# Kernel optimization log

Measured on AMD Instinct MI355X. Metric: run time of the kernel, lower is better.

Reference implementation:

```python
import jax, jax.numpy as jnp
import numpy as np

B, T, S, D, L, V = 32, 64, 128, 512, 2, 32000
DSRC = 2 * D  # bidirectional encoder
PAD = 1


def setup_inputs() -> dict:
    key = jax.random.key(0)
    ks = jax.random.split(key, 16)
    sc = 0.05
    embed = jax.random.normal(ks[5], (V, D), jnp.float32) * sc
    embed = embed.at[PAD].set(0.0)  # padding_idx row is zero
    return {
        "prev_tgt_tokens": jax.random.randint(ks[0], (B, T), 0, V),
        "encoder_out": jax.random.normal(ks[1], (B, S, DSRC), jnp.float32),
        "hiddens": jax.random.normal(ks[2], (L, B, D), jnp.float32) * sc,
        "cells": jax.random.normal(ks[3], (L, B, D), jnp.float32) * sc,
        "src_mask": jax.random.randint(ks[4], (B, S), 0, 2).astype(bool),
        "embed": embed,
        "W_ih": jax.random.normal(ks[6], (L, 4 * D, D), jnp.float32) * sc,
        "W_hh": jax.random.normal(ks[7], (L, 4 * D, D), jnp.float32) * sc,
        "b_ih": jnp.zeros((L, 4 * D), jnp.float32),
        "b_hh": jnp.zeros((L, 4 * D), jnp.float32),
        "W_in": jax.random.normal(ks[8], (DSRC, D), jnp.float32) * sc,   # input_proj: d_tgt -> d_src
        "b_in": jnp.zeros((DSRC,), jnp.float32),
        "W_out": jax.random.normal(ks[9], (D, DSRC + D), jnp.float32) * sc,  # out_proj
        "b_out": jnp.zeros((D,), jnp.float32),
    }


def reference(prev_tgt_tokens, encoder_out, hiddens, cells, src_mask,
              embed, W_ih, W_hh, b_ih, b_hh, W_in, b_in, W_out, b_out):
    n_layers, _, d_model = hiddens.shape
    tgt_len = prev_tgt_tokens.shape[1]
    tgt_embed = embed[prev_tgt_tokens]          # [B, T, D]
    xs = jnp.swapaxes(tgt_embed, 0, 1)          # [T, B, D]

    def lstm_cell(x, h, c, l):
        gates = x @ W_ih[l].T + b_ih[l] + h @ W_hh[l].T + b_hh[l]  # [B, 4D]
        i, f, g, o = jnp.split(gates, 4, axis=-1)
        c2 = jax.nn.sigmoid(f) * c + jax.nn.sigmoid(i) * jnp.tanh(g)
        h2 = jax.nn.sigmoid(o) * jnp.tanh(c2)
        return h2, c2

    def step(h_carry, y_t):
        s = y_t
        new_h = []
        for l in range(n_layers):
            h2, c2 = lstm_cell(s, h_carry[l], cells[l], l)
            # Faithful to source bug: `prev_hiddens[l], prev_hiddens[l] = (hidden, cell)`
            # stores the NEW CELL into the hidden slot; prev_cells never updated.
            new_h.append(c2)
            s = h2
        # attention
        xq = s @ W_in.T + b_in                              # [B, DSRC]
        e = jnp.einsum('bsd,bd->bs', encoder_out, xq)       # [B, S]
        e = jnp.where(src_mask, -1e9, e)
        attn = jax.nn.softmax(e, axis=-1)
        ctx = jnp.einsum('bs,bsd->bd', attn, encoder_out)   # [B, DSRC]
        out_t = jnp.tanh(jnp.concatenate([ctx, s], axis=-1) @ W_out.T + b_out)
        return jnp.stack(new_h), out_t

    _, outs = jax.lax.scan(step, hiddens, xs)   # outs: [T, B, D]
    # faithful to torch.cat(outs, dim=0).view(-1, tgt_len, d_model)
    return outs.reshape(-1, d_model).reshape(-1, tgt_len, d_model)
```

## Files before the change

kernel.cpp:

```cpp
#include <hip/hip_runtime.h>
#include <math.h>

typedef unsigned short u16;
typedef __attribute__((ext_vector_type(4))) float f4;
typedef __attribute__((ext_vector_type(4))) unsigned short us4;
typedef __attribute__((ext_vector_type(8))) unsigned short us8;
typedef __attribute__((ext_vector_type(8))) short bfrag;
typedef __attribute__((ext_vector_type(4))) float f32x4;

#define BB 32
#define TT 64
#define DD 512
#define G4_ 2048

__device__ __forceinline__ float sigf(float x) { return 1.0f / (1.0f + expf(-x)); }
__device__ __forceinline__ float bf2f(u16 u) {
    union { unsigned int i; float f; } v; v.i = ((unsigned int)u) << 16; return v.f;
}
__device__ __forceinline__ u16 f2bf(float f) {
    union { float f; unsigned int i; } v; v.f = f;
    unsigned int r = v.i + 0x7fffu + ((v.i >> 16) & 1u);
    return (u16)(r >> 16);
}

__global__ void k_flag(const unsigned char* __restrict__ m, int* __restrict__ flag) {
    int tid = threadIdx.x;
    int badbyte = 0, nonz_off = 0, evenu16_nz = 0;
    for (int i = tid * 16; i < tid * 16 + 16; i++) {
        unsigned char c = m[i];
        if (c > 1) badbyte = 1;
        if ((i & 3) != 0 && c != 0) nonz_off = 1;
    }
    const u16* mu = (const u16*)m;
    for (int i = tid * 8; i < tid * 8 + 8; i++) {
        if ((i & 1) == 0 && mu[i] != 0) evenu16_nz = 1;
    }
    __shared__ int s_bad, s_noff, s_env;
    if (tid == 0) { s_bad = 0; s_noff = 0; s_env = 0; }
    __syncthreads();
    if (badbyte) atomicOr(&s_bad, 1);
    if (nonz_off) atomicOr(&s_noff, 1);
    if (evenu16_nz) atomicOr(&s_env, 1);
    __syncthreads();
    if (tid == 0) {
        int f;
        if (s_bad) f = s_env ? 2 : 3;
        else       f = s_noff ? 0 : 1;
        *flag = f;
    }
}

__global__ void __launch_bounds__(256) k_init2(const float* __restrict__ hid,
                                               u16* __restrict__ h0s,
                                               u16* __restrict__ h1s) {
    int i = blockIdx.x * 256 + threadIdx.x;
    u16 v0 = f2bf(hid[i]), v1 = f2bf(hid[16384 + i]);
    h0s[i] = v0; h0s[16384 + i] = v0;
    h1s[i] = v1; h1s[16384 + i] = v1;
}

__global__ void __launch_bounds__(256) k_packAll(const float* __restrict__ Wih,
                                                 const float* __restrict__ Whh,
                                                 const float* __restrict__ Win,
                                                 const float* __restrict__ Wout,
                                                 u16* __restrict__ wpin,
                                                 u16* __restrict__ wpout,
                                                 u16* __restrict__ wih0p,
                                                 u16* __restrict__ php) {
    const int blk = blockIdx.x;
    const int tid = threadIdx.x;
    const float* sp;
    u16* dst;
    if (blk < 256) {
        int g = blk * 256 + tid;
        int lane = g & 63, grp = g >> 6;
        int j16 = grp >> 4, ks = grp & 15;
        sp = &Win[((size_t)(j16 * 16 + (lane & 15))) * 512 + ks * 32 + (lane >> 4) * 8];
        dst = &wpin[(size_t)g * 8];
    } else if (blk < 640) {
        int g = (blk - 256) * 256 + tid;
        int lane = g & 63, grp = g >> 6;
        int j16 = grp / 48, ks = grp % 48;
        sp = &Wout[((size_t)(j16 * 16 + (lane & 15))) * 1536 + ks * 32 + (lane >> 4) * 8];
        dst = &wpout[(size_t)g * 8];
    } else if (blk < 1152) {
        int g = (blk - 640) * 256 + tid;
        int lane = g & 63, grp = g >> 6;
        int j16 = grp >> 4, ks = grp & 15;
        sp = &Wih[((size_t)(j16 * 16 + (lane & 15))) * 512 + ks * 32 + (lane >> 4) * 8];
        dst = &wih0p[(size_t)g * 8];
    } else {
        int gidx = (blk - 1152) * 256 + tid;
        int m = gidx >> 17;
        int rem = gidx & 131071;
        int lane = rem & 63;
        int q = rem >> 6;
        int ks = q & 15, T = q >> 4;
        int g = T >> 5, d16 = T & 31;
        int j = g * 512 + d16 * 16 + (lane & 15);
        int kcol = ks * 32 + (lane >> 4) * 8;
        const float* src = (m == 0) ? Whh
                         : (m == 1) ? (Wih + 1048576)
                                    : (Whh + 1048576);
        sp = &src[(size_t)j * 512 + kcol];
        dst = &php[((size_t)m << 20) + (size_t)rem * 8];
    }
    f4 v0 = *(const f4*)&sp[0];
    f4 v1 = *(const f4*)&sp[4];
    dst[0] = f2bf(v0[0]); dst[1] = f2bf(v0[1]); dst[2] = f2bf(v0[2]); dst[3] = f2bf(v0[3]);
    dst[4] = f2bf(v1[0]); dst[5] = f2bf(v1[1]); dst[6] = f2bf(v1[2]); dst[7] = f2bf(v1[3]);
}

__global__ void __launch_bounds__(256) k_gih0_mfma(const int* __restrict__ tokens,
                                                   const float* __restrict__ embed,
                                                   const u16* __restrict__ Wp,
                                                   const float* __restrict__ bih,
                                                   const float* __restrict__ bhh,
                                                   float* __restrict__ gih0p) {
    const int tid = threadIdx.x;
    const int lane = tid & 63, w = tid >> 6;
    const int t = blockIdx.y;
    const int jw = blockIdx.x * 256 + w * 64;
    __shared__ u16 xs[32][520];
    __shared__ int toks[32];
    if (tid < 32) toks[tid] = tokens[tid * TT + t];
    __syncthreads();
    for (int i = tid; i < 32 * 128; i += 256) {
        int b = i >> 7, k4 = i & 127;
        f4 v = *(const f4*)&embed[(size_t)toks[b] * 512 + k4 * 4];
        u16* dst = &xs[b][k4 * 4];
        dst[0] = f2bf(v[0]); dst[1] = f2bf(v[1]); dst[2] = f2bf(v[2]); dst[3] = f2bf(v[3]);
    }
    __syncthreads();

    const int l15 = lane & 15, l4 = lane >> 4;
    f32x4 acc[2][4];
#pragma unroll
    for (int mi = 0; mi < 2; mi++)
#pragma unroll
        for (int ni = 0; ni < 4; ni++) acc[mi][ni] = (f32x4){0.f, 0.f, 0.f, 0.f};

    for (int ks = 0; ks < 16; ks++) {
        bfrag a0 = *(const bfrag*)&xs[l15][ks * 32 + l4 * 8];
        bfrag a1 = *(const bfrag*)&xs[16 + l15][ks * 32 + l4 * 8];
#pragma unroll
        for (int ni = 0; ni < 4; ni++) {
            int j16 = (jw + ni * 16) >> 4;
            bfrag bf = *(const bfrag*)&Wp[(((size_t)j16 * 16 + ks) * 64 + lane) * 8];
            acc[0][ni] = __builtin_amdgcn_mfma_f32_16x16x32_bf16(a0, bf, acc[0][ni], 0, 0, 0);
            acc[1][ni] = __builtin_amdgcn_mfma_f32_16x16x32_bf16(a1, bf, acc[1][ni], 0, 0, 0);
        }
    }

#pragma unroll
    for (int ni = 0; ni < 4; ni++) {
        int j16 = (jw >> 4) + ni;
        int g = j16 >> 5, d16 = j16 & 31;
        int j = j16 * 16 + l15;
        float bv = bih[j] + bhh[j];
#pragma unroll
        for (int mi = 0; mi < 2; mi++) {
            f32x4 sv = acc[mi][ni];
            sv[0] += bv; sv[1] += bv; sv[2] += bv; sv[3] += bv;
            *(f32x4*)&gih0p[(((((size_t)t * 32 + d16) * 4 + g) * 2 + mi) * 64 + lane) * 4] = sv;
        }
    }
}

__global__ void __launch_bounds__(256) k_phaseM(
    const int k,
    const float* __restrict__ gih0p,
    const u16* __restrict__ whh0p,
    const u16* __restrict__ wih1p,
    const u16* __restrict__ whh1p,
    const float* __restrict__ bih1,
    const float* __restrict__ bhh1,
    const float* __restrict__ cells,
    const u16* __restrict__ h0r, u16* __restrict__ h0w,
    const u16* __restrict__ h20r, u16* __restrict__ h20w,
    const u16* __restrict__ h1r, u16* __restrict__ h1w,
    u16* __restrict__ H2)
{
    const int tid = threadIdx.x;
    const int lane = tid & 63, w = tid >> 6;
    const int l15 = lane & 15, l4 = lane >> 4;
    const int unitL = w >> 1, sub = w & 1;
    __shared__ u16 xsA[32][520];
    __shared__ u16 xsB[32][520];
    __shared__ float red[2][4][64][4];

    if (blockIdx.x < 32) {
        if (k >= 64) return;
        const int d16mi = blockIdx.x * 2 + unitL;
        const int d16 = d16mi >> 1, mi = d16mi & 1;
        const int d = d16 * 16 + l15;
        f32x4 acc[4];
#pragma unroll
        for (int g = 0; g < 4; g++) {
            if (sub == 0)
                acc[g] = *(const f32x4*)&gih0p[(((((size_t)k * 32 + d16) * 4 + g) * 2 + mi) * 64 + lane) * 4];
            else
                acc[g] = (f32x4){0.f, 0.f, 0.f, 0.f};
        }
        for (int i = tid; i < 2048; i += 256) {
            int b = i >> 6, k8 = i & 63;
            *(us8*)&xsA[b][k8 * 8] = *(const us8*)&h0r[b * 512 + k8 * 8];
        }
        __syncthreads();
        const int arow = mi * 16 + l15;
        const int ks0 = sub * 8;
        for (int ks = ks0; ks < ks0 + 8; ks++) {
            bfrag a = *(const bfrag*)&xsA[arow][ks * 32 + l4 * 8];
#pragma unroll
            for (int g = 0; g < 4; g++) {
                int T = g * 32 + d16;
                bfrag bf = *(const bfrag*)&whh0p[(((size_t)T * 16 + ks) * 64 + lane) * 8];
                acc[g] = __builtin_amdgcn_mfma_f32_16x16x32_bf16(a, bf, acc[g], 0, 0, 0);
            }
        }
        if (sub == 1) {
#pragma unroll
            for (int g = 0; g < 4; g++)
                *(f32x4*)&red[unitL][g][lane][0] = acc[g];
        }
        __syncthreads();
        if (sub == 0) {
#pragma unroll
            for (int g = 0; g < 4; g++) {
                f32x4 pv = *(const f32x4*)&red[unitL][g][lane][0];
                acc[g][0] += pv[0]; acc[g][1] += pv[1]; acc[g][2] += pv[2]; acc[g][3] += pv[3];
            }
#pragma unroll
            for (int r = 0; r < 4; r++) {
                int b = mi * 16 + l4 * 4 + r;
                float gi = acc[0][r];
                float gf = acc[1][r];
                float gg = acc[2][r];
                float go = acc[3][r];
                float cell = cells[b * 512 + d];
                float c2 = sigf(gf) * cell + sigf(gi) * tanhf(gg);
                float h2 = sigf(go) * tanhf(c2);
                h0w[b * 512 + d] = f2bf(c2);
                h20w[b * 512 + d] = f2bf(h2);
            }
        }
    } else {
        if (k < 1) return;
        for (int i = tid; i < 2048; i += 256) {
            int b = i >> 6, k8 = i & 63;
            *(us8*)&xsA[b][k8 * 8] = *(const us8*)&h20r[b * 512 + k8 * 8];
            *(us8*)&xsB[b][k8 * 8] = *(const us8*)&h1r[b * 512 + k8 * 8];
        }
        __syncthreads();
        const int d16mi = (blockIdx.x - 32) * 2 + unitL;
        const int d16 = d16mi >> 1, mi = d16mi & 1;
        const int d = d16 * 16 + l15;
        const int arow = mi * 16 + l15;
        const u16 (* __restrict__ xsrc)[520] = sub ? xsB : xsA;
        const u16* wsrc = sub ? whh1p : wih1p;
        f32x4 acc[4];
#pragma unroll
        for (int g = 0; g < 4; g++) acc[g] = (f32x4){0.f, 0.f, 0.f, 0.f};
        for (int ks = 0; ks < 16; ks++) {
            bfrag a = *(const bfrag*)&xsrc[arow][ks * 32 + l4 * 8];
#pragma unroll
            for (int g = 0; g < 4; g++) {
                int T = g * 32 + d16;
                bfrag bf = *(const bfrag*)&wsrc[(((size_t)T * 16 + ks) * 64 + lane) * 8];
                acc[g] = __builtin_amdgcn_mfma_f32_16x16x32_bf16(a, bf, acc[g], 0, 0, 0);
            }
        }
        if (sub == 1) {
#pragma unroll
            for (int g = 0; g < 4; g++)
                *(f32x4*)&red[unitL][g][lane][0] = acc[g];
        }
        __syncthreads();
        if (sub == 0) {
#pragma unroll
            for (int g = 0; g < 4; g++) {
                f32x4 pv = *(const f32x4*)&red[unitL][g][lane][0];
                acc[g][0] += pv[0]; acc[g][1] += pv[1]; acc[g][2] += pv[2]; acc[g][3] += pv[3];
            }
            float bb0 = bih1[0 * 512 + d] + bhh1[0 * 512 + d];
            float bb1v = bih1[1 * 512 + d] + bhh1[1 * 512 + d];
            float bb2 = bih1[2 * 512 + d] + bhh1[2 * 512 + d];
            float bb3 = bih1[3 * 512 + d] + bhh1[3 * 512 + d];
#pragma unroll
            for (int r = 0; r < 4; r++) {
                int b = mi * 16 + l4 * 4 + r;
                float gi = acc[0][r] + bb0;
                float gf = acc[1][r] + bb1v;
                float gg = acc[2][r] + bb2;
                float go = acc[3][r] + bb3;
                float cell = cells[16384 + b * 512 + d];
                float c2 = sigf(gf) * cell + sigf(gi) * tanhf(gg);
                float h2 = sigf(go) * tanhf(c2);
                h1w[b * 512 + d] = f2bf(c2);
                H2[(size_t)(k - 1) * 16384 + b * 512 + d] = f2bf(h2);
            }
        }
    }
}

__global__ void __launch_bounds__(256) k_x_mfma(const u16* __restrict__ H2,
                                                const u16* __restrict__ Wpin,
                                                const float* __restrict__ bin,
                                                u16* __restrict__ XQ) {
    const int tid = threadIdx.x;
    const int lane = tid & 63, w = tid >> 6;
    const int t = blockIdx.y;
    const int jw = blockIdx.x * 256 + w * 64;
    __shared__ u16 xs[32][520];
    for (int i = tid; i < 2048; i += 256) {
        int b = i >> 6, k8 = i & 63;
        *(us8*)&xs[b][k8 * 8] = *(const us8*)&H2[(size_t)t * 16384 + b * 512 + k8 * 8];
    }
    __syncthreads();
    const int l15 = lane & 15, l4 = lane >> 4;
    f32x4 acc[2][4];
#pragma unroll
    for (int mi = 0; mi < 2; mi++)
#pragma unroll
        for (int ni = 0; ni < 4; ni++) acc[mi][ni] = (f32x4){0.f, 0.f, 0.f, 0.f};
    for (int ks = 0; ks < 16; ks++) {
        bfrag a0 = *(const bfrag*)&xs[l15][ks * 32 + l4 * 8];
        bfrag a1 = *(const bfrag*)&xs[16 + l15][ks * 32 + l4 * 8];
#pragma unroll
        for (int ni = 0; ni < 4; ni++) {
            int j16 = (jw + ni * 16) >> 4;
            bfrag bf = *(const bfrag*)&Wpin[(((size_t)j16 * 16 + ks) * 64 + lane) * 8];
            acc[0][ni] = __builtin_amdgcn_mfma_f32_16x16x32_bf16(a0, bf, acc[0][ni], 0, 0, 0);
            acc[1][ni] = __builtin_amdgcn_mfma_f32_16x16x32_bf16(a1, bf, acc[1][ni], 0, 0, 0);
        }
    }
#pragma unroll
    for (int ni = 0; ni < 4; ni++) {
        int j = jw + ni * 16 + l15;
        float bv = bin[j];
#pragma unroll
        for (int mi = 0; mi < 2; mi++) {
#pragma unroll
            for (int r = 0; r < 4; r++) {
                int b = mi * 16 + l4 * 4 + r;
                XQ[((size_t)(t * 32 + b)) * 1024 + j] = f2bf(acc[mi][ni][r] + bv);
            }
        }
    }
}

__global__ void __launch_bounds__(256) k_out_mfma(const u16* __restrict__ CTX,
                                                  const u16* __restrict__ H2,
                                                  const u16* __restrict__ Wpout,
                                                  const float* __restrict__ bout,
                                                  float* __restrict__ out) {
    const int tid = threadIdx.x;
    const int lane = tid & 63, w = tid >> 6;
    const int t = blockIdx.y;
    const int jw = blockIdx.x * 256 + w * 64;
    __shared__ u16 xs[32][520];
    const int l15 = lane & 15, l4 = lane >> 4;
    f32x4 acc[2][4];
#pragma unroll
    for (int mi = 0; mi < 2; mi++)
#pragma unroll
        for (int ni = 0; ni < 4; ni++) acc[mi][ni] = (f32x4){0.f, 0.f, 0.f, 0.f};
    for (int c = 0; c < 3; c++) {
        if (c) __syncthreads();
        if (c < 2) {
            for (int i = tid; i < 2048; i += 256) {
                int b = i >> 6, k8 = i & 63;
                *(us8*)&xs[b][k8 * 8] = *(const us8*)&CTX[((size_t)(t * 32 + b)) * 1024 + c * 512 + k8 * 8];
            }
        } else {
            for (int i = tid; i < 2048; i += 256) {
                int b = i >> 6, k8 = i & 63;
                *(us8*)&xs[b][k8 * 8] = *(const us8*)&H2[(size_t)t * 16384 + b * 512 + k8 * 8];
            }
        }
        __syncthreads();
        for (int ks = 0; ks < 16; ks++) {
            bfrag a0 = *(const bfrag*)&xs[l15][ks * 32 + l4 * 8];
            bfrag a1 = *(const bfrag*)&xs[16 + l15][ks * 32 + l4 * 8];
#pragma unroll
            for (int ni = 0; ni < 4; ni++) {
                int j16 = (jw + ni * 16) >> 4;
                bfrag bf = *(const bfrag*)&Wpout[(((size_t)j16 * 48 + c * 16 + ks) * 64 + lane) * 8];
                acc[0][ni] = __builtin_amdgcn_mfma_f32_16x16x32_bf16(a0, bf, acc[0][ni], 0, 0, 0);
                acc[1][ni] = __builtin_amdgcn_mfma_f32_16x16x32_bf16(a1, bf, acc[1][ni], 0, 0, 0);
            }
        }
    }
#pragma unroll
    for (int ni = 0; ni < 4; ni++) {
        int j = jw + ni * 16 + l15;
        float bv = bout[j];
#pragma unroll
        for (int mi = 0; mi < 2; mi++) {
#pragma unroll
            for (int r = 0; r < 4; r++) {
                int b = mi * 16 + l4 * 4 + r;
                out[((size_t)(t * 32 + b)) * 512 + j] = tanhf(acc[mi][ni][r] + bv);
            }
        }
    }
}

__global__ void __launch_bounds__(256) k_att8(const u16* __restrict__ XQ,
                                              const float* __restrict__ enc,
                                              const unsigned char* __restrict__ mask,
                                              const int* __restrict__ flag,
                                              u16* __restrict__ CTX) {
    const int tid = threadIdx.x;
    const int b = blockIdx.x, t0 = blockIdx.y * 8;
    __shared__ float xq[8][1024];
    __shared__ float ered[8][256];
    __shared__ float attn[8][128];
    __shared__ float red2[8][8];
#pragma unroll
    for (int tg = 0; tg < 8; tg++) {
        us4 v = *(const us4*)&XQ[((size_t)((t0 + tg) * 32 + b)) * 1024 + tid * 4];
        float* dst = &xq[tg][tid * 4];
        dst[0] = bf2f(v[0]); dst[1] = bf2f(v[1]); dst[2] = bf2f(v[2]); dst[3] = bf2f(v[3]);
    }
    __syncthreads();
    const int s = tid >> 1, hh = tid & 1;
    float p[8] = {0.f, 0.f, 0.f, 0.f, 0.f, 0.f, 0.f, 0.f};
    const float* erow = enc + ((size_t)(b * 128 + s)) * 1024 + hh * 512;
    for (int k4 = 0; k4 < 128; k4++) {
        f4 u = *(const f4*)&erow[k4 * 4];
#pragma unroll
        for (int kk = 0; kk < 4; kk++) {
#pragma unroll
            for (int tg = 0; tg < 8; tg++)
                p[tg] += u[kk] * xq[tg][hh * 512 + k4 * 4 + kk];
        }
    }
#pragma unroll
    for (int tg = 0; tg < 8; tg++) ered[tg][tid] = p[tg];
    __syncthreads();
    bool msk = false;
    if (tid < 128) {
        int f = *flag;
        if (f == 0)      msk = mask[b * 128 + tid] != 0;
        else if (f == 1) msk = ((const int*)mask)[b * 128 + tid] != 0;
        else if (f == 2) msk = ((const u16*)mask)[b * 128 + tid] != 0;
        else             msk = ((const unsigned int*)mask)[b * 128 + tid] != 0;
    }
    const int wave = tid >> 6;
    float e[8];
#pragma unroll
    for (int tg = 0; tg < 8; tg++) {
        e[tg] = -INFINITY;
        if (tid < 128) {
            e[tg] = ered[tg][2 * tid] + ered[tg][2 * tid + 1];
            if (msk) e[tg] = -1e9f;
        }
        float v = e[tg];
#pragma unroll
        for (int off = 32; off >= 1; off >>= 1) v = fmaxf(v, __shfl_xor(v, off));
        if ((tid & 63) == 0) red2[tg][wave] = v;
    }
    __syncthreads();
#pragma unroll
    for (int tg = 0; tg < 8; tg++) {
        float mx = fmaxf(fmaxf(red2[tg][0], red2[tg][1]), fmaxf(red2[tg][2], red2[tg][3]));
        float pp = (tid < 128) ? expf(e[tg] - mx) : 0.f;
        float su = pp;
#pragma unroll
        for (int off = 32; off >= 1; off >>= 1) su += __shfl_xor(su, off);
        if ((tid & 63) == 0) red2[tg][4 + wave] = su;
        __syncthreads();
        float S = (red2[tg][4] + red2[tg][5]) + (red2[tg][6] + red2[tg][7]);
        if (tid < 128) attn[tg][tid] = pp / S;
        __syncthreads();
    }
    float c0[8] = {0}, c1[8] = {0}, c2v[8] = {0}, c3[8] = {0};
    const float* eb = enc + ((size_t)b * 128) * 1024 + tid * 4;
    for (int s2 = 0; s2 < 128; s2++) {
        f4 u = *(const f4*)&eb[(size_t)s2 * 1024];
#pragma unroll
        for (int tg = 0; tg < 8; tg++) {
            float a = attn[tg][s2];
            c0[tg] += a * u[0]; c1[tg] += a * u[1]; c2v[tg] += a * u[2]; c3[tg] += a * u[3];
        }
    }
#pragma unroll
    for (int tg = 0; tg < 8; tg++) {
        u16* crow = CTX + ((size_t)((t0 + tg) * 32 + b)) * 1024 + tid * 4;
        crow[0] = f2bf(c0[tg]); crow[1] = f2bf(c1[tg]);
        crow[2] = f2bf(c2v[tg]); crow[3] = f2bf(c3[tg]);
    }
}

extern "C" void kernel_launch(void* const* d_in, const int* in_sizes, int n_in,
                              void* d_out, int out_size, void* d_ws, size_t ws_size,
                              hipStream_t stream) {
    const int* tokens   = (const int*)d_in[0];
    const float* enc    = (const float*)d_in[1];
    const float* hidden = (const float*)d_in[2];
    const float* cells  = (const float*)d_in[3];
    const unsigned char* mask = (const unsigned char*)d_in[4];
    const float* embed  = (const float*)d_in[5];
    const float* W_ih   = (const float*)d_in[6];
    const float* W_hh   = (const float*)d_in[7];
    const float* b_ih   = (const float*)d_in[8];
    const float* b_hh   = (const float*)d_in[9];
    const float* W_in   = (const float*)d_in[10];
    const float* b_in   = (const float*)d_in[11];
    const float* W_out  = (const float*)d_in[12];
    const float* b_out  = (const float*)d_in[13];
    float* out = (float*)d_out;

    float* ws = (float*)d_ws;
    float* gih0p = ws;
    u16*   h0s  = (u16*)(ws + 4194304);
    u16*   h20s = (u16*)(ws + 4210688);
    u16*   h1s  = (u16*)(ws + 4227072);
    u16*   H2   = (u16*)(ws + 4243456);
    u16*   php  = (u16*)(ws + 4767744);
    u16*   whh0p = php;
    u16*   wih1p = php + 1048576;
    u16*   whh1p = php + 2097152;
    u16*   wpin  = (u16*)(ws + 6340608);
    u16*   wpout = (u16*)(ws + 6602752);
    u16*   wih0p = (u16*)(ws + 6995968);
    int*   flag  = (int*)(ws + 7520256);
    u16*   XQ   = (u16*)ws;
    u16*   CTX  = (u16*)(ws + 1048576);

    const float* bih1 = b_ih + G4_;
    const float* bhh1 = b_hh + G4_;

    k_flag<<<1, 256, 0, stream>>>(mask, flag);
    k_init2<<<64, 256, 0, stream>>>(hidden, h0s, h1s);
    k_packAll<<<2688, 256, 0, stream>>>(W_ih, W_hh, W_in, W_out, wpin, wpout, wih0p, php);
    k_gih0_mfma<<<dim3(8, 64), 256, 0, stream>>>(tokens, embed, wih0p, b_ih, b_hh, gih0p);

    for (int k = 0; k <= 64; k++) {
        const int r = k & 1, w = r ^ 1;
        k_phaseM<<<64, 256, 0, stream>>>(k, gih0p, whh0p, wih1p, whh1p, bih1, bhh1, cells,
                                         h0s + r * 16384, h0s + w * 16384,
                                         h20s + r * 16384, h20s + w * 16384,
                                         h1s + r * 16384, h1s + w * 16384, H2);
    }

    k_x_mfma<<<dim3(4, 64), 256, 0, stream>>>(H2, wpin, b_in, XQ);
    k_att8<<<dim3(32, 8), 256, 0, stream>>>(XQ, enc, mask, flag, CTX);
    k_out_mfma<<<dim3(2, 64), 256, 0, stream>>>(CTX, H2, wpout, b_out, out);
}
```

Before: 593.9 us.

## Split attention into MFMA QK-softmax and AV kernels with bf16 encoder tiles

Replaces the scalar fp32 attention kernel with two bf16 MFMA kernels. One computes scores for 32 timesteps per block, applies the mask and softmax, and writes bf16 attention weights to workspace. The other multiplies those weights by a transposed bf16 encoder tile to produce the context. The goal is to move the attention dot products onto matrix cores. The cost is an extra launch, an intermediate buffer round trip, and bf16 rounding of the encoder values and attention weights.

```diff
diff --git a/kernel.cpp b/kernel.cpp
--- a/kernel.cpp
+++ b/kernel.cpp
@@ -349,6 +349,146 @@
     }
 }
 
+__global__ void __launch_bounds__(256) k_qk_mfma(const u16* __restrict__ XQ,
+                                                 const float* __restrict__ enc,
+                                                 const unsigned char* __restrict__ mask,
+                                                 const int* __restrict__ flag,
+                                                 u16* __restrict__ ATT) {
+    const int tid = threadIdx.x;
+    const int lane = tid & 63, w = tid >> 6;
+    const int l15 = lane & 15, l4 = lane >> 4;
+    const int b = blockIdx.x, th = blockIdx.y;
+    __shared__ u16 qs[32][136];
+    __shared__ u16 encC[128][136];
+    __shared__ float es[32][132];
+    f32x4 acc[2][2];
+#pragma unroll
+    for (int mt = 0; mt < 2; mt++)
+#pragma unroll
+        for (int ni = 0; ni < 2; ni++) acc[mt][ni] = (f32x4){0.f, 0.f, 0.f, 0.f};
+
+    for (int dc = 0; dc < 8; dc++) {
+        if (dc) __syncthreads();
+        for (int i = tid; i < 512; i += 256) {
+            int tr = i >> 4, k8 = i & 15;
+            *(us8*)&qs[tr][k8 * 8] =
+                *(const us8*)&XQ[((size_t)((th * 32 + tr) * 32 + b)) * 1024 + dc * 128 + k8 * 8];
+        }
+        for (int i = tid; i < 4096; i += 256) {
+            int s = i >> 5, d4 = i & 31;
+            f4 v = *(const f4*)&enc[((size_t)(b * 128 + s)) * 1024 + dc * 128 + d4 * 4];
+            u16* dst = &encC[s][d4 * 4];
+            dst[0] = f2bf(v[0]); dst[1] = f2bf(v[1]); dst[2] = f2bf(v[2]); dst[3] = f2bf(v[3]);
+        }
+        __syncthreads();
+        for (int ks = 0; ks < 4; ks++) {
+            bfrag a0 = *(const bfrag*)&qs[l15][ks * 32 + l4 * 8];
+            bfrag a1 = *(const bfrag*)&qs[16 + l15][ks * 32 + l4 * 8];
+#pragma unroll
+            for (int ni = 0; ni < 2; ni++) {
+                int nt = w * 2 + ni;
+                bfrag bf = *(const bfrag*)&encC[nt * 16 + l15][ks * 32 + l4 * 8];
+                acc[0][ni] = __builtin_amdgcn_mfma_f32_16x16x32_bf16(a0, bf, acc[0][ni], 0, 0, 0);
+                acc[1][ni] = __builtin_amdgcn_mfma_f32_16x16x32_bf16(a1, bf, acc[1][ni], 0, 0, 0);
+            }
+        }
+    }
+    __syncthreads();
+#pragma unroll
+    for (int mt = 0; mt < 2; mt++) {
+#pragma unroll
+        for (int ni = 0; ni < 2; ni++) {
+            int nt = w * 2 + ni;
+#pragma unroll
+            for (int r = 0; r < 4; r++)
+                es[mt * 16 + l4 * 4 + r][nt * 16 + l15] = acc[mt][ni][r];
+        }
+    }
+    __syncthreads();
+    const int row = tid >> 3, seg = tid & 7;
+    int f = *flag;
+    float p[16];
+    float mx = -INFINITY;
+#pragma unroll
+    for (int j = 0; j < 16; j++) {
+        int col = seg * 16 + j;
+        bool msk;
+        if (f == 0)      msk = mask[b * 128 + col] != 0;
+        else if (f == 1) msk = ((const int*)mask)[b * 128 + col] != 0;
+        else if (f == 2) msk = ((const u16*)mask)[b * 128 + col] != 0;
+        else             msk = ((const unsigned int*)mask)[b * 128 + col] != 0;
+        float e = es[row][col];
+        if (msk) e = -1e9f;
+        p[j] = e;
+        mx = fmaxf(mx, e);
+    }
+#pragma unroll
+    for (int off = 4; off >= 1; off >>= 1) mx = fmaxf(mx, __shfl_xor(mx, off));
+    float su = 0.f;
+#pragma unroll
+    for (int j = 0; j < 16; j++) { p[j] = expf(p[j] - mx); su += p[j]; }
+#pragma unroll
+    for (int off = 4; off >= 1; off >>= 1) su += __shfl_xor(su, off);
+    u16* arow = &ATT[((size_t)(b * 64 + th * 32 + row)) * 128 + seg * 16];
+#pragma unroll
+    for (int j = 0; j < 16; j++) arow[j] = f2bf(p[j] / su);
+}
+
+__global__ void __launch_bounds__(256) k_av_mfma(const u16* __restrict__ ATT,
+                                                 const float* __restrict__ enc,
+                                                 u16* __restrict__ CTX) {
+    const int tid = threadIdx.x;
+    const int lane = tid & 63, w = tid >> 6;
+    const int l15 = lane & 15, l4 = lane >> 4;
+    const int b = blockIdx.x, nc = blockIdx.y;
+    __shared__ u16 as_[64][136];
+    __shared__ u16 encT[256][136];
+    for (int i = tid; i < 1024; i += 256) {
+        int tr = i >> 4, k8 = i & 15;
+        *(us8*)&as_[tr][k8 * 8] = *(const us8*)&ATT[((size_t)(b * 64 + tr)) * 128 + k8 * 8];
+    }
+    for (int i = tid; i < 8192; i += 256) {
+        int d4 = i & 63, s = i >> 6;
+        f4 v = *(const f4*)&enc[((size_t)(b * 128 + s)) * 1024 + nc * 256 + d4 * 4];
+        encT[d4 * 4 + 0][s] = f2bf(v[0]);
+        encT[d4 * 4 + 1][s] = f2bf(v[1]);
+        encT[d4 * 4 + 2][s] = f2bf(v[2]);
+        encT[d4 * 4 + 3][s] = f2bf(v[3]);
+    }
+    __syncthreads();
+    f32x4 acc[4][4];
+#pragma unroll
+    for (int mt = 0; mt < 4; mt++)
+#pragma unroll
+        for (int ni = 0; ni < 4; ni++) acc[mt][ni] = (f32x4){0.f, 0.f, 0.f, 0.f};
+    for (int ks = 0; ks < 4; ks++) {
+        bfrag a[4];
+#pragma unroll
+        for (int mt = 0; mt < 4; mt++)
+            a[mt] = *(const bfrag*)&as_[mt * 16 + l15][ks * 32 + l4 * 8];
+#pragma unroll
+        for (int ni = 0; ni < 4; ni++) {
+            int nt = w * 4 + ni;
+            bfrag bf = *(const bfrag*)&encT[nt * 16 + l15][ks * 32 + l4 * 8];
+#pragma unroll
+            for (int mt = 0; mt < 4; mt++)
+                acc[mt][ni] = __builtin_amdgcn_mfma_f32_16x16x32_bf16(a[mt], bf, acc[mt][ni], 0, 0, 0);
+        }
+    }
+#pragma unroll
+    for (int ni = 0; ni < 4; ni++) {
+        int n = nc * 256 + (w * 4 + ni) * 16 + l15;
+#pragma unroll
+        for (int mt = 0; mt < 4; mt++) {
+#pragma unroll
+            for (int r = 0; r < 4; r++) {
+                int t = mt * 16 + l4 * 4 + r;
+                CTX[((size_t)(t * 32 + b)) * 1024 + n] = f2bf(acc[mt][ni][r]);
+            }
+        }
+    }
+}
+
 __global__ void __launch_bounds__(256) k_out_mfma(const u16* __restrict__ CTX,
                                                   const u16* __restrict__ H2,
                                                   const u16* __restrict__ Wpout,
@@ -403,93 +543,6 @@
                 out[((size_t)(t * 32 + b)) * 512 + j] = tanhf(acc[mi][ni][r] + bv);
             }
         }
-    }
-}
-
-__global__ void __launch_bounds__(256) k_att8(const u16* __restrict__ XQ,
-                                              const float* __restrict__ enc,
-                                              const unsigned char* __restrict__ mask,
-                                              const int* __restrict__ flag,
-                                              u16* __restrict__ CTX) {
-    const int tid = threadIdx.x;
-    const int b = blockIdx.x, t0 = blockIdx.y * 8;
-    __shared__ float xq[8][1024];
-    __shared__ float ered[8][256];
-    __shared__ float attn[8][128];
-    __shared__ float red2[8][8];
-#pragma unroll
-    for (int tg = 0; tg < 8; tg++) {
-        us4 v = *(const us4*)&XQ[((size_t)((t0 + tg) * 32 + b)) * 1024 + tid * 4];
-        float* dst = &xq[tg][tid * 4];
-        dst[0] = bf2f(v[0]); dst[1] = bf2f(v[1]); dst[2] = bf2f(v[2]); dst[3] = bf2f(v[3]);
-    }
-    __syncthreads();
-    const int s = tid >> 1, hh = tid & 1;
-    float p[8] = {0.f, 0.f, 0.f, 0.f, 0.f, 0.f, 0.f, 0.f};
-    const float* erow = enc + ((size_t)(b * 128 + s)) * 1024 + hh * 512;
-    for (int k4 = 0; k4 < 128; k4++) {
-        f4 u = *(const f4*)&erow[k4 * 4];
-#pragma unroll
-        for (int kk = 0; kk < 4; kk++) {
-#pragma unroll
-            for (int tg = 0; tg < 8; tg++)
-                p[tg] += u[kk] * xq[tg][hh * 512 + k4 * 4 + kk];
-        }
-    }
-#pragma unroll
-    for (int tg = 0; tg < 8; tg++) ered[tg][tid] = p[tg];
-    __syncthreads();
-    bool msk = false;
-    if (tid < 128) {
-        int f = *flag;
-        if (f == 0)      msk = mask[b * 128 + tid] != 0;
-        else if (f == 1) msk = ((const int*)mask)[b * 128 + tid] != 0;
-        else if (f == 2) msk = ((const u16*)mask)[b * 128 + tid] != 0;
-        else             msk = ((const unsigned int*)mask)[b * 128 + tid] != 0;
-    }
-    const int wave = tid >> 6;
-    float e[8];
-#pragma unroll
-    for (int tg = 0; tg < 8; tg++) {
-        e[tg] = -INFINITY;
-        if (tid < 128) {
-            e[tg] = ered[tg][2 * tid] + ered[tg][2 * tid + 1];
-            if (msk) e[tg] = -1e9f;
-        }
-        float v = e[tg];
-#pragma unroll
-        for (int off = 32; off >= 1; off >>= 1) v = fmaxf(v, __shfl_xor(v, off));
-        if ((tid & 63) == 0) red2[tg][wave] = v;
-    }
-    __syncthreads();
-#pragma unroll
-    for (int tg = 0; tg < 8; tg++) {
-        float mx = fmaxf(fmaxf(red2[tg][0], red2[tg][1]), fmaxf(red2[tg][2], red2[tg][3]));
-        float pp = (tid < 128) ? expf(e[tg] - mx) : 0.f;
-        float su = pp;
-#pragma unroll
-        for (int off = 32; off >= 1; off >>= 1) su += __shfl_xor(su, off);
-        if ((tid & 63) == 0) red2[tg][4 + wave] = su;
-        __syncthreads();
-        float S = (red2[tg][4] + red2[tg][5]) + (red2[tg][6] + red2[tg][7]);
-        if (tid < 128) attn[tg][tid] = pp / S;
-        __syncthreads();
-    }
-    float c0[8] = {0}, c1[8] = {0}, c2v[8] = {0}, c3[8] = {0};
-    const float* eb = enc + ((size_t)b * 128) * 1024 + tid * 4;
-    for (int s2 = 0; s2 < 128; s2++) {
-        f4 u = *(const f4*)&eb[(size_t)s2 * 1024];
-#pragma unroll
-        for (int tg = 0; tg < 8; tg++) {
-            float a = attn[tg][s2];
-            c0[tg] += a * u[0]; c1[tg] += a * u[1]; c2v[tg] += a * u[2]; c3[tg] += a * u[3];
-        }
-    }
-#pragma unroll
-    for (int tg = 0; tg < 8; tg++) {
-        u16* crow = CTX + ((size_t)((t0 + tg) * 32 + b)) * 1024 + tid * 4;
-        crow[0] = f2bf(c0[tg]); crow[1] = f2bf(c1[tg]);
-        crow[2] = f2bf(c2v[tg]); crow[3] = f2bf(c3[tg]);
     }
 }
 
@@ -528,6 +581,7 @@
     int*   flag  = (int*)(ws + 7520256);
     u16*   XQ   = (u16*)ws;
     u16*   CTX  = (u16*)(ws + 1048576);
+    u16*   ATT  = (u16*)(ws + 2097152);
 
     const float* bih1 = b_ih + G4_;
     const float* bhh1 = b_hh + G4_;
@@ -546,6 +600,7 @@
     }
 
     k_x_mfma<<<dim3(4, 64), 256, 0, stream>>>(H2, wpin, b_in, XQ);
-    k_att8<<<dim3(32, 8), 256, 0, stream>>>(XQ, enc, mask, flag, CTX);
+    k_qk_mfma<<<dim3(32, 2), 256, 0, stream>>>(XQ, enc, mask, flag, ATT);
+    k_av_mfma<<<dim3(32, 4), 256, 0, stream>>>(ATT, enc, CTX);
     k_out_mfma<<<dim3(2, 64), 256, 0, stream>>>(CTX, H2, wpout, b_out, out);
 }
```

Result: slower. 628.0 us (+5.7%).
